# Kernel tuning notes

Measured on AMD Instinct MI355X. Metric: run time of the kernel, lower is better.

## Reference

```python
import jax, jax.numpy as jnp
import numpy as np

D_MODEL = 1024
HIDDEN = 4096
NUM_EXPERTS = 8
NUM_GROUPS = 4      # from _compute_group_size(4, 4096) with max_group_size=4096
GROUP_SIZE = 4096
EXPERT_CAPACITY = 512  # round(1.0 * 4096 / 8), >= max(8, 4096//100)


def setup_inputs() -> dict:
    key = jax.random.key(0)
    ks = jax.random.split(key, 10)
    s_in = 1.0 / np.sqrt(D_MODEL)
    s_hid = 1.0 / np.sqrt(HIDDEN)
    return {
        "x": jax.random.normal(ks[0], (4, 4096, D_MODEL), dtype=jnp.float32),
        "gate_w": jax.random.normal(ks[1], (D_MODEL, NUM_EXPERTS), dtype=jnp.float32) * 0.1,
        "gate_b": jax.random.normal(ks[2], (NUM_EXPERTS,), dtype=jnp.float32) * 0.01,
        "temperature": jnp.ones((1,), dtype=jnp.float32),
        "shared_w1": jax.random.normal(ks[3], (D_MODEL, HIDDEN), dtype=jnp.float32) * s_in,
        "shared_b1": jnp.zeros((HIDDEN,), dtype=jnp.float32),
        "shared_w2": jax.random.normal(ks[4], (HIDDEN, D_MODEL), dtype=jnp.float32) * s_hid,
        "shared_b2": jnp.zeros((D_MODEL,), dtype=jnp.float32),
        "expert_w1": jax.random.normal(ks[5], (NUM_EXPERTS, D_MODEL, HIDDEN), dtype=jnp.float32) * s_in,
        "expert_b1": jnp.zeros((NUM_EXPERTS, HIDDEN), dtype=jnp.float32),
        "expert_w2": jax.random.normal(ks[6], (NUM_EXPERTS, HIDDEN, D_MODEL), dtype=jnp.float32) * s_hid,
        "expert_b2": jnp.zeros((NUM_EXPERTS, D_MODEL), dtype=jnp.float32),
    }


def reference(x, gate_w, gate_b, temperature, shared_w1, shared_b1, shared_w2,
              shared_b2, expert_w1, expert_b1, expert_w2, expert_b2):
    B, S, D = x.shape
    T = NUM_GROUPS * GROUP_SIZE  # total tokens (no padding here)
    xg = x.reshape(NUM_GROUPS, GROUP_SIZE, D)

    # Router: softmax over temperature-scaled gate logits
    logits = jnp.einsum('gsd,de->gse', xg, gate_w) + gate_b
    safe_temp = jnp.maximum(temperature, 0.1)
    probs = jax.nn.softmax(logits / safe_temp, axis=-1)  # [G, Gs, E]
    # per-expert top-k over ALL tokens (flattened across groups)
    flat_probs = probs.transpose(2, 0, 1).reshape(NUM_EXPERTS, T)
    scores, tok_idx = jax.lax.top_k(flat_probs, EXPERT_CAPACITY)  # [E, C]

    # Shared expert FFN (gelu is tanh-approx, matching flax nn.gelu default)
    shared = jnp.einsum('gsh,hd->gsd',
                        jax.nn.gelu(jnp.einsum('gsd,dh->gsh', xg, shared_w1) + shared_b1),
                        shared_w2) + shared_b2

    # Routed experts: gather tokens, grouped FFN, weighted scatter-add
    x_flat = xg.reshape(T, D)
    tokens = x_flat[tok_idx]  # [E, C, D]
    h = jax.nn.gelu(jnp.einsum('ecd,edh->ech', tokens, expert_w1) + expert_b1[:, None, :])
    out_e = jnp.einsum('ech,ehd->ecd', h, expert_w2) + expert_b2[:, None, :]
    out_e = out_e * scores[..., None]
    routed = jnp.zeros_like(x_flat).at[tok_idx.reshape(-1)].add(out_e.reshape(-1, D))

    out = shared.reshape(T, D) + routed
    return out.reshape(B, S, D)
```

## Files before the change

kernel.cpp:

```cpp
#include <hip/hip_runtime.h>

#define NTOK 16384
#define DMODEL 1024
#define DHID 4096
#define NEXP 8
#define CAP 512

typedef __attribute__((ext_vector_type(8))) short bfrag_t;
typedef __attribute__((ext_vector_type(4))) float ffrag_t;

__device__ __forceinline__ unsigned short f2bf(float f) {
  unsigned u = __float_as_uint(f);
  u += 0x7FFFu + ((u >> 16) & 1u);
  return (unsigned short)(u >> 16);
}

__device__ __forceinline__ float gelu_fast(float x) {
  float t = x * x;
  float z = x * fmaf(0.071354814f, t, 1.5957691f);
  float e = __expf(-z);
  return x * __builtin_amdgcn_rcpf(1.0f + e);
}

__global__ void k_convert_bf16(const float* __restrict__ in, unsigned short* __restrict__ out, int n4) {
  int i = blockIdx.x * blockDim.x + threadIdx.x;
  int stride = gridDim.x * blockDim.x;
  for (; i < n4; i += stride) {
    float4 v = ((const float4*)in)[i];
    ushort4 o;
    o.x = f2bf(v.x); o.y = f2bf(v.y); o.z = f2bf(v.z); o.w = f2bf(v.w);
    ((ushort4*)out)[i] = o;
  }
}

__global__ void k_trans_conv(const float* __restrict__ in, unsigned short* __restrict__ out, int K, int N) {
  const size_t zb = blockIdx.z;
  in  += zb * (size_t)K * N;
  out += zb * (size_t)N * K;
  __shared__ float tile[32][33];
  const int n0 = blockIdx.x * 32, k0 = blockIdx.y * 32;
  const int tx = threadIdx.x & 31, ty = threadIdx.x >> 5;
#pragma unroll
  for (int i = 0; i < 4; ++i) {
    int k = ty + i * 8;
    tile[k][tx] = in[(size_t)(k0 + k) * N + n0 + tx];
  }
  __syncthreads();
#pragma unroll
  for (int i = 0; i < 4; ++i) {
    int n = ty + i * 8;
    out[(size_t)(n0 + n) * K + k0 + tx] = f2bf(tile[tx][n]);
  }
}

__global__ __launch_bounds__(256) void k_router(const float* __restrict__ x, const float* __restrict__ gw,
                                                const float* __restrict__ gb, const float* __restrict__ temp,
                                                float* __restrict__ probs) {
  __shared__ float gws[DMODEL * NEXP];
  for (int i = threadIdx.x; i < DMODEL * NEXP; i += 256) gws[i] = gw[i];
  __syncthreads();
  const int wave = threadIdx.x >> 6, lane = threadIdx.x & 63;
  const int t = blockIdx.x * 4 + wave;
  const float* xr = x + (size_t)t * DMODEL;
  float acc[NEXP];
#pragma unroll
  for (int e = 0; e < NEXP; ++e) acc[e] = 0.f;
  for (int d = lane; d < DMODEL; d += 64) {
    float xv = xr[d];
#pragma unroll
    for (int e = 0; e < NEXP; ++e) acc[e] += xv * gws[d * NEXP + e];
  }
#pragma unroll
  for (int off = 32; off >= 1; off >>= 1) {
#pragma unroll
    for (int e = 0; e < NEXP; ++e) acc[e] += __shfl_xor(acc[e], off);
  }
  if (lane == 0) {
    float st = fmaxf(temp[0], 0.1f);
    float m = -1e30f;
#pragma unroll
    for (int e = 0; e < NEXP; ++e) { acc[e] = (acc[e] + gb[e]) / st; m = fmaxf(m, acc[e]); }
    float s = 0.f;
#pragma unroll
    for (int e = 0; e < NEXP; ++e) { acc[e] = expf(acc[e] - m); s += acc[e]; }
    float inv = 1.f / s;
#pragma unroll
    for (int e = 0; e < NEXP; ++e) probs[(size_t)e * NTOK + t] = acc[e] * inv;
  }
}

__global__ __launch_bounds__(256) void k_topk(const float* __restrict__ probs, int* __restrict__ tok,
                                              float* __restrict__ scores, int* __restrict__ eqbuf) {
  const int e = blockIdx.x;
  const float* p = probs + (size_t)e * NTOK;
  int* eq = eqbuf + (size_t)e * NTOK;
  __shared__ int hist[256];
  __shared__ unsigned sh_pref;
  __shared__ int sh_k, sh_gt, sh_eq, sh_cnt;
  const int tid = threadIdx.x;
  if (tid == 0) { sh_pref = 0u; sh_k = CAP; }
  __syncthreads();
  for (int pass = 3; pass >= 0; --pass) {
    hist[tid] = 0;
    __syncthreads();
    const unsigned pref = sh_pref;
    const int shift = pass * 8;
    for (int t = tid; t < NTOK; t += 256) {
      unsigned key = __float_as_uint(p[t]);
      bool cand = (pass == 3) || ((key >> (shift + 8)) == pref);
      if (cand) atomicAdd(&hist[(key >> shift) & 255], 1);
    }
    __syncthreads();
    if (tid == 0) {
      int k = sh_k;
      int d = 255;
      while (hist[d] < k) { k -= hist[d]; --d; }
      sh_k = k;
      sh_pref = (pref << 8) | (unsigned)d;
    }
    __syncthreads();
  }
  const unsigned Kstar = sh_pref;
  const int need_eq = sh_k;
  if (tid == 0) { sh_gt = 0; sh_eq = 0; }
  __syncthreads();
  for (int t = tid; t < NTOK; t += 256) {
    unsigned key = __float_as_uint(p[t]);
    if (key > Kstar) {
      int pos = atomicAdd(&sh_gt, 1);
      tok[e * CAP + pos] = t;
      scores[e * CAP + pos] = p[t];
    } else if (key == Kstar) {
      int q = atomicAdd(&sh_eq, 1);
      eq[q] = t;
    }
  }
  __syncthreads();
  const int cg = sh_gt, ce = sh_eq;
  if (ce <= need_eq) {
    for (int j = tid; j < ce; j += 256) {
      tok[e * CAP + cg + j] = eq[j];
      scores[e * CAP + cg + j] = p[eq[j]];
    }
  } else {
    int lo = 0, hi = NTOK - 1;
    while (lo < hi) {
      int mid = (lo + hi) >> 1;
      if (tid == 0) sh_cnt = 0;
      __syncthreads();
      for (int j = tid; j < ce; j += 256)
        if (eq[j] <= mid) atomicAdd(&sh_cnt, 1);
      __syncthreads();
      if (sh_cnt >= need_eq) hi = mid; else lo = mid + 1;
      __syncthreads();
    }
    if (tid == 0) sh_cnt = 0;
    __syncthreads();
    for (int j = tid; j < ce; j += 256) {
      if (eq[j] <= lo) {
        int pos = cg + atomicAdd(&sh_cnt, 1);
        tok[e * CAP + pos] = eq[j];
        scores[e * CAP + pos] = p[eq[j]];
      }
    }
  }
}

__global__ void k_gather(const unsigned short* __restrict__ xb, const int* __restrict__ tok,
                         unsigned short* __restrict__ atok) {
  const int row = blockIdx.x;
  const int t = tok[row];
  const uint2* src = (const uint2*)(xb + (size_t)t * DMODEL);
  uint2* dst = (uint2*)(atok + (size_t)row * DMODEL);
  dst[threadIdx.x] = src[threadIdx.x];
}

template <int MODE>
__global__ __launch_bounds__(256, 4) void k_gemm(
    const unsigned short* __restrict__ A, const unsigned short* __restrict__ Bt,
    const float* __restrict__ bias, float* __restrict__ outF, unsigned short* __restrict__ outB,
    const int* __restrict__ tok, const float* __restrict__ scale,
    int M, int N, int Kloop, int LDK, int ksplit) {
  const int zb = blockIdx.z / ksplit;
  const int kc = blockIdx.z % ksplit;
  A += (size_t)zb * M * LDK + (size_t)kc * Kloop;
  Bt += (size_t)zb * N * LDK + (size_t)kc * Kloop;
  const float* bz = bias + (size_t)zb * N;

  const int gx = gridDim.x, gy = gridDim.y;
  const int nwg = gx * gy;
  const int id = blockIdx.x + blockIdx.y * gx;
  int bx, by;
  if ((gx & 7) == 0) {
    const int x = id & 7, c = id >> 3, H = gx >> 3;
    bx = x * H + (c % H);
    by = c / H;
  } else if ((nwg & 7) == 0) {
    const int q = nwg >> 3;
    const int sw = (id & 7) * q + (id >> 3);
    bx = sw % gx;
    by = sw / gx;
  } else {
    bx = blockIdx.x;
    by = blockIdx.y;
  }
  const int m0 = bx * 128, n0 = by * 128;

  const int tid = threadIdx.x, wave = tid >> 6, lane = tid & 63;
  const int wm = (wave >> 1) * 64, wn = (wave & 1) * 64;

  __shared__ alignas(16) unsigned short sh[128 * 128];
  unsigned short* As = sh;
  unsigned short* Bs = sh + 128 * 64;

  ffrag_t acc[4][4];
#pragma unroll
  for (int i = 0; i < 4; ++i)
#pragma unroll
    for (int j = 0; j < 4; ++j)
#pragma unroll
      for (int r = 0; r < 4; ++r) acc[i][j][r] = 0.f;

  int rr[4], gg[4], lb[4];
#pragma unroll
  for (int it = 0; it < 4; ++it) {
    int L = it * 256 + tid;
    rr[it] = L >> 3;
    gg[it] = (L & 7) ^ (rr[it] & 7);
    lb[it] = (it * 256 + wave * 64) * 16;
  }

  for (int kt = 0; kt < Kloop; kt += 64) {
#pragma unroll
    for (int it = 0; it < 4; ++it) {
      const unsigned short* sA = A + (size_t)(m0 + rr[it]) * LDK + kt + gg[it] * 8;
      const unsigned short* sB = Bt + (size_t)(n0 + rr[it]) * LDK + kt + gg[it] * 8;
      __builtin_amdgcn_global_load_lds((const __attribute__((address_space(1))) unsigned int*)sA,
                                       (__attribute__((address_space(3))) unsigned int*)((char*)As + lb[it]),
                                       16, 0, 0);
      __builtin_amdgcn_global_load_lds((const __attribute__((address_space(1))) unsigned int*)sB,
                                       (__attribute__((address_space(3))) unsigned int*)((char*)Bs + lb[it]),
                                       16, 0, 0);
    }
    __syncthreads();
#pragma unroll
    for (int kk = 0; kk < 2; ++kk) {
      bfrag_t af[4], bf[4];
      const int gl = kk * 4 + (lane >> 4);
#pragma unroll
      for (int mi = 0; mi < 4; ++mi) {
        int r = wm + mi * 16 + (lane & 15);
        af[mi] = *(const bfrag_t*)&As[r * 64 + ((gl ^ (r & 7)) * 8)];
      }
#pragma unroll
      for (int ni = 0; ni < 4; ++ni) {
        int r = wn + ni * 16 + (lane & 15);
        bf[ni] = *(const bfrag_t*)&Bs[r * 64 + ((gl ^ (r & 7)) * 8)];
      }
#pragma unroll
      for (int mi = 0; mi < 4; ++mi)
#pragma unroll
        for (int ni = 0; ni < 4; ++ni)
          acc[mi][ni] = __builtin_amdgcn_mfma_f32_16x16x32_bf16(af[mi], bf[ni], acc[mi][ni], 0, 0, 0);
    }
    __syncthreads();
  }

  const int rsub = (lane >> 4) * 4, cs = lane & 15;
  if (MODE == 0) {
    float bv[4];
#pragma unroll
    for (int ni = 0; ni < 4; ++ni) bv[ni] = bz[n0 + wn + ni * 16 + cs];
#pragma unroll
    for (int mi = 0; mi < 4; ++mi)
#pragma unroll
      for (int ni = 0; ni < 4; ++ni)
#pragma unroll
        for (int r = 0; r < 4; ++r) {
          float v = acc[mi][ni][r] + bv[ni];
          sh[(wm + mi * 16 + rsub + r) * 128 + (wn + ni * 16 + cs)] = f2bf(gelu_fast(v));
        }
    __syncthreads();
    const int seg = tid & 15, rw = tid >> 4;
#pragma unroll
    for (int rep = 0; rep < 8; ++rep) {
      const int row = rep * 16 + rw;
      uint4 v = *(const uint4*)&sh[row * 128 + seg * 8];
      *(uint4*)&outB[((size_t)zb * M + m0 + row) * N + n0 + seg * 8] = v;
    }
  } else if (MODE == 1) {
#pragma unroll
    for (int ni = 0; ni < 4; ++ni) {
      const int n = n0 + wn + ni * 16 + cs;
      const float bv = bz[n];
#pragma unroll
      for (int mi = 0; mi < 4; ++mi)
#pragma unroll
        for (int r = 0; r < 4; ++r) {
          const int m = m0 + wm + mi * 16 + rsub + r;
          outF[(size_t)m * N + n] = acc[mi][ni][r] + bv;
        }
    }
  } else {
#pragma unroll
    for (int ni = 0; ni < 4; ++ni) {
      const int n = n0 + wn + ni * 16 + cs;
      const float bv = (kc == 0) ? bz[n] : 0.f;
#pragma unroll
      for (int mi = 0; mi < 4; ++mi)
#pragma unroll
        for (int r = 0; r < 4; ++r) {
          const int m = m0 + wm + mi * 16 + rsub + r;
          const int t = tok[zb * M + m];
          const float s = scale[zb * M + m];
          atomicAdd(&outF[(size_t)t * N + n], (acc[mi][ni][r] + bv) * s);
        }
    }
  }
}

extern "C" void kernel_launch(void* const* d_in, const int* in_sizes, int n_in,
                              void* d_out, int out_size, void* d_ws, size_t ws_size,
                              hipStream_t stream) {
  const float* x      = (const float*)d_in[0];
  const float* gate_w = (const float*)d_in[1];
  const float* gate_b = (const float*)d_in[2];
  const float* temp   = (const float*)d_in[3];
  const float* sw1    = (const float*)d_in[4];
  const float* sb1    = (const float*)d_in[5];
  const float* sw2    = (const float*)d_in[6];
  const float* sb2    = (const float*)d_in[7];
  const float* ew1    = (const float*)d_in[8];
  const float* eb1    = (const float*)d_in[9];
  const float* ew2    = (const float*)d_in[10];
  const float* eb2    = (const float*)d_in[11];
  float* out = (float*)d_out;

  char* ws = (char*)d_ws;
  size_t o = 0;
  auto take = [&](size_t bytes) { char* p = ws + o; o += (bytes + 255) & ~(size_t)255; return p; };
  unsigned short* x_bf = (unsigned short*)take((size_t)NTOK * DMODEL * 2);
  unsigned short* w1t  = (unsigned short*)take((size_t)DMODEL * DHID * 2);
  unsigned short* w2t  = (unsigned short*)take((size_t)DHID * DMODEL * 2);
  unsigned short* ew1t = (unsigned short*)take((size_t)NEXP * DMODEL * DHID * 2);
  unsigned short* ew2t = (unsigned short*)take((size_t)NEXP * DHID * DMODEL * 2);
  float* probs         = (float*)take((size_t)NEXP * NTOK * 4);
  int* tok             = (int*)take((size_t)NEXP * CAP * 4);
  float* scores        = (float*)take((size_t)NEXP * CAP * 4);
  int* eqbuf           = (int*)take((size_t)NEXP * NTOK * 4);
  unsigned short* atok = (unsigned short*)take((size_t)NEXP * CAP * DMODEL * 2);
  unsigned short* he   = (unsigned short*)take((size_t)NEXP * CAP * DHID * 2);
  unsigned short* hs   = (unsigned short*)take((size_t)NTOK * DHID * 2);

  k_convert_bf16<<<4096, 256, 0, stream>>>(x, x_bf, NTOK * DMODEL / 4);
  k_trans_conv<<<dim3(DHID / 32, DMODEL / 32, 1), 256, 0, stream>>>(sw1, w1t, DMODEL, DHID);
  k_trans_conv<<<dim3(DMODEL / 32, DHID / 32, 1), 256, 0, stream>>>(sw2, w2t, DHID, DMODEL);
  k_trans_conv<<<dim3(DHID / 32, DMODEL / 32, NEXP), 256, 0, stream>>>(ew1, ew1t, DMODEL, DHID);
  k_trans_conv<<<dim3(DMODEL / 32, DHID / 32, NEXP), 256, 0, stream>>>(ew2, ew2t, DHID, DMODEL);

  k_router<<<NTOK / 4, 256, 0, stream>>>(x, gate_w, gate_b, temp, probs);
  k_topk<<<NEXP, 256, 0, stream>>>(probs, tok, scores, eqbuf);
  k_gather<<<NEXP * CAP, 256, 0, stream>>>(x_bf, tok, atok);

  k_gemm<0><<<dim3(128, 32, 1), 256, 0, stream>>>(
      x_bf, w1t, sb1, nullptr, hs, nullptr, nullptr, NTOK, DHID, DMODEL, DMODEL, 1);
  k_gemm<1><<<dim3(128, 8, 1), 256, 0, stream>>>(
      hs, w2t, sb2, out, nullptr, nullptr, nullptr, NTOK, DMODEL, DHID, DHID, 1);

  k_gemm<0><<<dim3(4, 32, NEXP), 256, 0, stream>>>(
      atok, ew1t, eb1, nullptr, he, nullptr, nullptr, CAP, DHID, DMODEL, DMODEL, 1);
  k_gemm<2><<<dim3(4, 8, NEXP * 4), 256, 0, stream>>>(
      he, ew2t, eb2, out, nullptr, tok, scores, CAP, DMODEL, DHID / 4, DHID, 4);
}
```

Baseline: 700.8 us.

## Fuse x conversion into router, gather in GEMM, replace atomic scatter with combine

```diff
diff --git a/kernel.cpp b/kernel.cpp
--- a/kernel.cpp
+++ b/kernel.cpp
@@ -22,51 +22,49 @@
   return x * __builtin_amdgcn_rcpf(1.0f + e);
 }
 
-__global__ void k_convert_bf16(const float* __restrict__ in, unsigned short* __restrict__ out, int n4) {
-  int i = blockIdx.x * blockDim.x + threadIdx.x;
-  int stride = gridDim.x * blockDim.x;
-  for (; i < n4; i += stride) {
-    float4 v = ((const float4*)in)[i];
-    ushort4 o;
-    o.x = f2bf(v.x); o.y = f2bf(v.y); o.z = f2bf(v.z); o.w = f2bf(v.w);
-    ((ushort4*)out)[i] = o;
-  }
-}
-
-__global__ void k_trans_conv(const float* __restrict__ in, unsigned short* __restrict__ out, int K, int N) {
+__global__ __launch_bounds__(256) void k_trans64(const float* __restrict__ in,
+                                                 unsigned short* __restrict__ out, int K, int N) {
   const size_t zb = blockIdx.z;
   in  += zb * (size_t)K * N;
   out += zb * (size_t)N * K;
-  __shared__ float tile[32][33];
-  const int n0 = blockIdx.x * 32, k0 = blockIdx.y * 32;
-  const int tx = threadIdx.x & 31, ty = threadIdx.x >> 5;
-#pragma unroll
-  for (int i = 0; i < 4; ++i) {
-    int k = ty + i * 8;
+  __shared__ float tile[64][65];
+  const int n0 = blockIdx.x * 64, k0 = blockIdx.y * 64;
+  const int tx = threadIdx.x & 63, ty = threadIdx.x >> 6;
+#pragma unroll
+  for (int i = 0; i < 16; ++i) {
+    const int k = ty * 16 + i;
     tile[k][tx] = in[(size_t)(k0 + k) * N + n0 + tx];
   }
   __syncthreads();
-#pragma unroll
-  for (int i = 0; i < 4; ++i) {
-    int n = ty + i * 8;
-    out[(size_t)(n0 + n) * K + k0 + tx] = f2bf(tile[tx][n]);
+  const int sx = threadIdx.x & 7, sy = threadIdx.x >> 3;
+#pragma unroll
+  for (int j = 0; j < 2; ++j) {
+    const int n = sy + j * 32;
+    uint4 v;
+    v.x = (unsigned)f2bf(tile[sx * 8 + 0][n]) | ((unsigned)f2bf(tile[sx * 8 + 1][n]) << 16);
+    v.y = (unsigned)f2bf(tile[sx * 8 + 2][n]) | ((unsigned)f2bf(tile[sx * 8 + 3][n]) << 16);
+    v.z = (unsigned)f2bf(tile[sx * 8 + 4][n]) | ((unsigned)f2bf(tile[sx * 8 + 5][n]) << 16);
+    v.w = (unsigned)f2bf(tile[sx * 8 + 6][n]) | ((unsigned)f2bf(tile[sx * 8 + 7][n]) << 16);
+    *(uint4*)&out[(size_t)(n0 + n) * K + k0 + sx * 8] = v;
   }
 }
 
 __global__ __launch_bounds__(256) void k_router(const float* __restrict__ x, const float* __restrict__ gw,
                                                 const float* __restrict__ gb, const float* __restrict__ temp,
-                                                float* __restrict__ probs) {
+                                                float* __restrict__ probs, unsigned short* __restrict__ xb) {
   __shared__ float gws[DMODEL * NEXP];
   for (int i = threadIdx.x; i < DMODEL * NEXP; i += 256) gws[i] = gw[i];
   __syncthreads();
   const int wave = threadIdx.x >> 6, lane = threadIdx.x & 63;
   const int t = blockIdx.x * 4 + wave;
   const float* xr = x + (size_t)t * DMODEL;
+  unsigned short* xw = xb + (size_t)t * DMODEL;
   float acc[NEXP];
 #pragma unroll
   for (int e = 0; e < NEXP; ++e) acc[e] = 0.f;
   for (int d = lane; d < DMODEL; d += 64) {
     float xv = xr[d];
+    xw[d] = f2bf(xv);
 #pragma unroll
     for (int e = 0; e < NEXP; ++e) acc[e] += xv * gws[d * NEXP + e];
   }
@@ -90,14 +88,17 @@
 }
 
 __global__ __launch_bounds__(256) void k_topk(const float* __restrict__ probs, int* __restrict__ tok,
-                                              float* __restrict__ scores, int* __restrict__ eqbuf) {
+                                              float* __restrict__ scores, int* __restrict__ eqbuf,
+                                              int* __restrict__ slot) {
   const int e = blockIdx.x;
   const float* p = probs + (size_t)e * NTOK;
   int* eq = eqbuf + (size_t)e * NTOK;
+  int* sl = slot + (size_t)e * NTOK;
   __shared__ int hist[256];
   __shared__ unsigned sh_pref;
   __shared__ int sh_k, sh_gt, sh_eq, sh_cnt;
   const int tid = threadIdx.x;
+  for (int t = tid; t < NTOK; t += 256) sl[t] = -1;
   if (tid == 0) { sh_pref = 0u; sh_k = CAP; }
   __syncthreads();
   for (int pass = 3; pass >= 0; --pass) {
@@ -130,6 +131,7 @@
       int pos = atomicAdd(&sh_gt, 1);
       tok[e * CAP + pos] = t;
       scores[e * CAP + pos] = p[t];
+      sl[t] = pos;
     } else if (key == Kstar) {
       int q = atomicAdd(&sh_eq, 1);
       eq[q] = t;
@@ -141,6 +143,7 @@
     for (int j = tid; j < ce; j += 256) {
       tok[e * CAP + cg + j] = eq[j];
       scores[e * CAP + cg + j] = p[eq[j]];
+      sl[eq[j]] = cg + j;
     }
   } else {
     int lo = 0, hi = NTOK - 1;
@@ -161,21 +164,50 @@
         int pos = cg + atomicAdd(&sh_cnt, 1);
         tok[e * CAP + pos] = eq[j];
         scores[e * CAP + pos] = p[eq[j]];
+        sl[eq[j]] = pos;
       }
     }
   }
 }
 
-__global__ void k_gather(const unsigned short* __restrict__ xb, const int* __restrict__ tok,
-                         unsigned short* __restrict__ atok) {
-  const int row = blockIdx.x;
-  const int t = tok[row];
-  const uint2* src = (const uint2*)(xb + (size_t)t * DMODEL);
-  uint2* dst = (uint2*)(atok + (size_t)row * DMODEL);
-  dst[threadIdx.x] = src[threadIdx.x];
-}
-
-template <int MODE>
+__global__ __launch_bounds__(256) void k_combine(const float* __restrict__ pe,
+                                                 const int* __restrict__ slot,
+                                                 float* __restrict__ out) {
+  const int wave = threadIdx.x >> 6, lane = threadIdx.x & 63;
+  const int t = blockIdx.x * 4 + wave;
+  int sl[NEXP];
+  bool any = false;
+#pragma unroll
+  for (int e = 0; e < NEXP; ++e) {
+    sl[e] = slot[(size_t)e * NTOK + t];
+    any = any || (sl[e] >= 0);
+  }
+  if (!any) return;
+  float* orow = out + (size_t)t * DMODEL;
+  float4 a[4];
+#pragma unroll
+  for (int i = 0; i < 4; ++i) a[i] = *(float4*)&orow[i * 256 + lane * 4];
+#pragma unroll
+  for (int e = 0; e < NEXP; ++e) {
+    if (sl[e] >= 0) {
+      const float* p0 = pe + (((size_t)e * 2 + 0) * CAP + sl[e]) * DMODEL;
+      const float* p1 = pe + (((size_t)e * 2 + 1) * CAP + sl[e]) * DMODEL;
+#pragma unroll
+      for (int i = 0; i < 4; ++i) {
+        float4 v0 = *(const float4*)&p0[i * 256 + lane * 4];
+        float4 v1 = *(const float4*)&p1[i * 256 + lane * 4];
+        a[i].x += v0.x + v1.x;
+        a[i].y += v0.y + v1.y;
+        a[i].z += v0.z + v1.z;
+        a[i].w += v0.w + v1.w;
+      }
+    }
+  }
+#pragma unroll
+  for (int i = 0; i < 4; ++i) *(float4*)&orow[i * 256 + lane * 4] = a[i];
+}
+
+template <int MODE, bool GATHER>
 __global__ __launch_bounds__(256, 4) void k_gemm(
     const unsigned short* __restrict__ A, const unsigned short* __restrict__ Bt,
     const float* __restrict__ bias, float* __restrict__ outF, unsigned short* __restrict__ outB,
@@ -183,7 +215,8 @@
     int M, int N, int Kloop, int LDK, int ksplit) {
   const int zb = blockIdx.z / ksplit;
   const int kc = blockIdx.z % ksplit;
-  A += (size_t)zb * M * LDK + (size_t)kc * Kloop;
+  if (!GATHER) A += (size_t)zb * M * LDK;
+  A += (size_t)kc * Kloop;
   Bt += (size_t)zb * N * LDK + (size_t)kc * Kloop;
   const float* bz = bias + (size_t)zb * N;
 
@@ -221,26 +254,30 @@
 #pragma unroll
       for (int r = 0; r < 4; ++r) acc[i][j][r] = 0.f;
 
-  int rr[4], gg[4], lb[4];
+  int lb[4];
+  const unsigned short* rowA[4];
+  const unsigned short* rowB[4];
 #pragma unroll
   for (int it = 0; it < 4; ++it) {
     int L = it * 256 + tid;
-    rr[it] = L >> 3;
-    gg[it] = (L & 7) ^ (rr[it] & 7);
+    int rr = L >> 3;
+    int gg = (L & 7) ^ (rr & 7);
     lb[it] = (it * 256 + wave * 64) * 16;
+    const unsigned short* ab =
+        GATHER ? (A + (size_t)tok[zb * M + m0 + rr] * LDK) : (A + (size_t)(m0 + rr) * LDK);
+    rowA[it] = ab + gg * 8;
+    rowB[it] = Bt + (size_t)(n0 + rr) * LDK + gg * 8;
   }
 
   for (int kt = 0; kt < Kloop; kt += 64) {
 #pragma unroll
     for (int it = 0; it < 4; ++it) {
-      const unsigned short* sA = A + (size_t)(m0 + rr[it]) * LDK + kt + gg[it] * 8;
-      const unsigned short* sB = Bt + (size_t)(n0 + rr[it]) * LDK + kt + gg[it] * 8;
-      __builtin_amdgcn_global_load_lds((const __attribute__((address_space(1))) unsigned int*)sA,
-                                       (__attribute__((address_space(3))) unsigned int*)((char*)As + lb[it]),
-                                       16, 0, 0);
-      __builtin_amdgcn_global_load_lds((const __attribute__((address_space(1))) unsigned int*)sB,
-                                       (__attribute__((address_space(3))) unsigned int*)((char*)Bs + lb[it]),
-                                       16, 0, 0);
+      __builtin_amdgcn_global_load_lds(
+          (const __attribute__((address_space(1))) unsigned int*)(rowA[it] + kt),
+          (__attribute__((address_space(3))) unsigned int*)((char*)As + lb[it]), 16, 0, 0);
+      __builtin_amdgcn_global_load_lds(
+          (const __attribute__((address_space(1))) unsigned int*)(rowB[it] + kt),
+          (__attribute__((address_space(3))) unsigned int*)((char*)Bs + lb[it]), 16, 0, 0);
     }
     __syncthreads();
 #pragma unroll
@@ -302,6 +339,7 @@
         }
     }
   } else {
+    float* po = outF + (size_t)blockIdx.z * M * N;
 #pragma unroll
     for (int ni = 0; ni < 4; ++ni) {
       const int n = n0 + wn + ni * 16 + cs;
@@ -311,9 +349,8 @@
 #pragma unroll
         for (int r = 0; r < 4; ++r) {
           const int m = m0 + wm + mi * 16 + rsub + r;
-          const int t = tok[zb * M + m];
           const float s = scale[zb * M + m];
-          atomicAdd(&outF[(size_t)t * N + n], (acc[mi][ni][r] + bv) * s);
+          po[(size_t)m * N + n] = (acc[mi][ni][r] + bv) * s;
         }
     }
   }
@@ -348,27 +385,28 @@
   int* tok             = (int*)take((size_t)NEXP * CAP * 4);
   float* scores        = (float*)take((size_t)NEXP * CAP * 4);
   int* eqbuf           = (int*)take((size_t)NEXP * NTOK * 4);
-  unsigned short* atok = (unsigned short*)take((size_t)NEXP * CAP * DMODEL * 2);
+  int* slot            = (int*)take((size_t)NEXP * NTOK * 4);
+  float* pe            = (float*)take((size_t)NEXP * 2 * CAP * DMODEL * 4);
   unsigned short* he   = (unsigned short*)take((size_t)NEXP * CAP * DHID * 2);
   unsigned short* hs   = (unsigned short*)take((size_t)NTOK * DHID * 2);
 
-  k_convert_bf16<<<4096, 256, 0, stream>>>(x, x_bf, NTOK * DMODEL / 4);
-  k_trans_conv<<<dim3(DHID / 32, DMODEL / 32, 1), 256, 0, stream>>>(sw1, w1t, DMODEL, DHID);
-  k_trans_conv<<<dim3(DMODEL / 32, DHID / 32, 1), 256, 0, stream>>>(sw2, w2t, DHID, DMODEL);
-  k_trans_conv<<<dim3(DHID / 32, DMODEL / 32, NEXP), 256, 0, stream>>>(ew1, ew1t, DMODEL, DHID);
-  k_trans_conv<<<dim3(DMODEL / 32, DHID / 32, NEXP), 256, 0, stream>>>(ew2, ew2t, DHID, DMODEL);
-
-  k_router<<<NTOK / 4, 256, 0, stream>>>(x, gate_w, gate_b, temp, probs);
-  k_topk<<<NEXP, 256, 0, stream>>>(probs, tok, scores, eqbuf);
-  k_gather<<<NEXP * CAP, 256, 0, stream>>>(x_bf, tok, atok);
-
-  k_gemm<0><<<dim3(128, 32, 1), 256, 0, stream>>>(
+  k_trans64<<<dim3(DHID / 64, DMODEL / 64, 1), 256, 0, stream>>>(sw1, w1t, DMODEL, DHID);
+  k_trans64<<<dim3(DMODEL / 64, DHID / 64, 1), 256, 0, stream>>>(sw2, w2t, DHID, DMODEL);
+  k_trans64<<<dim3(DHID / 64, DMODEL / 64, NEXP), 256, 0, stream>>>(ew1, ew1t, DMODEL, DHID);
+  k_trans64<<<dim3(DMODEL / 64, DHID / 64, NEXP), 256, 0, stream>>>(ew2, ew2t, DHID, DMODEL);
+
+  k_router<<<NTOK / 4, 256, 0, stream>>>(x, gate_w, gate_b, temp, probs, x_bf);
+  k_topk<<<NEXP, 256, 0, stream>>>(probs, tok, scores, eqbuf, slot);
+
+  k_gemm<0, false><<<dim3(128, 32, 1), 256, 0, stream>>>(
       x_bf, w1t, sb1, nullptr, hs, nullptr, nullptr, NTOK, DHID, DMODEL, DMODEL, 1);
-  k_gemm<1><<<dim3(128, 8, 1), 256, 0, stream>>>(
+  k_gemm<1, false><<<dim3(128, 8, 1), 256, 0, stream>>>(
       hs, w2t, sb2, out, nullptr, nullptr, nullptr, NTOK, DMODEL, DHID, DHID, 1);
 
-  k_gemm<0><<<dim3(4, 32, NEXP), 256, 0, stream>>>(
-      atok, ew1t, eb1, nullptr, he, nullptr, nullptr, CAP, DHID, DMODEL, DMODEL, 1);
-  k_gemm<2><<<dim3(4, 8, NEXP * 4), 256, 0, stream>>>(
-      he, ew2t, eb2, out, nullptr, tok, scores, CAP, DMODEL, DHID / 4, DHID, 4);
-}
+  k_gemm<0, true><<<dim3(4, 32, NEXP), 256, 0, stream>>>(
+      x_bf, ew1t, eb1, nullptr, he, tok, nullptr, CAP, DHID, DMODEL, DMODEL, 1);
+  k_gemm<3, false><<<dim3(4, 8, NEXP * 2), 256, 0, stream>>>(
+      he, ew2t, eb2, pe, nullptr, nullptr, scores, CAP, DMODEL, DHID / 2, DHID, 2);
+
+  k_combine<<<NTOK / 4, 256, 0, stream>>>(pe, slot, out);
+}
```

Result: faster. 670.7 us (-4.3%).
